# Performance work log

Measured on AMD Instinct MI355X. Metric: run time of the kernel, lower is better.

Reference implementation:

```python
import jax, jax.numpy as jnp
import numpy as np

BITS = 4
MASK = (1 << BITS) - 1  # 15
GROUP_SIZE = 128
IN_F, OUT_F = 4096, 11008
N_GROUPS = IN_F // GROUP_SIZE  # 32
PACK = 32 // BITS  # 8 nibbles per int32


def setup_inputs() -> dict:
    key = jax.random.key(0)
    k1, k2, k3, k4, k5 = jax.random.split(key, 5)
    x = jax.random.normal(k1, (64, IN_F), dtype=jnp.float32)
    # arbitrary packed int4 payloads: random 32-bit patterns viewed as int32
    qweight = jax.lax.bitcast_convert_type(
        jax.random.bits(k2, (IN_F // 32 * BITS, OUT_F), dtype=jnp.uint32), jnp.int32)
    qzeros = jax.lax.bitcast_convert_type(
        jax.random.bits(k3, (N_GROUPS, OUT_F // 32 * BITS), dtype=jnp.uint32), jnp.int32)
    scales = (jax.random.uniform(k4, (N_GROUPS, OUT_F), dtype=jnp.float32) + 0.1) * 0.01
    g_idx = (jnp.arange(IN_F, dtype=jnp.int32) // GROUP_SIZE).astype(jnp.int32)
    bias = jax.random.normal(k5, (OUT_F,), dtype=jnp.float32)
    return {"x": x, "qweight": qweight, "qzeros": qzeros,
            "scales": scales, "g_idx": g_idx, "bias": bias}


def reference(x, qweight, qzeros, scales, g_idx, bias):
    wf = jnp.arange(0, 32, BITS, dtype=jnp.int32)  # [8] shift amounts
    # unpack zero points: [n_groups, out/8, 8] -> [n_groups, out]
    zeros = (jnp.right_shift(qzeros[:, :, None], wf[None, None, :]) & MASK) + 1
    zeros = zeros.reshape(scales.shape).astype(scales.dtype)
    # unpack weights: [in/8, 8, out] -> [in, out]
    w = jnp.right_shift(qweight[:, None, :], wf[None, :, None]) & MASK
    w = w.reshape(-1, qweight.shape[1]).astype(scales.dtype)
    # per-group dequant, then dense matmul
    W = scales[g_idx] * (w - zeros[g_idx])  # [in, out]
    out = jnp.matmul(x, W).astype(x.dtype) + bias.astype(x.dtype)
    return out
```

## Files before the change

### kernel.cpp

```cpp
#include <hip/hip_runtime.h>

#define IN_F 4096
#define OUT_F 11008
#define M_ROWS 64
#define KSPLIT 4
#define GPB 8
#define NT_BLK 64
#define NBLK_N (OUT_F / NT_BLK)
#define QZ_WORDS (OUT_F / 8)
#define LDS_ROW 65

typedef __attribute__((ext_vector_type(8))) short short8;
typedef __attribute__((ext_vector_type(4))) float float4v;

__device__ __forceinline__ short f2bf(float f) {
    unsigned u = __builtin_bit_cast(unsigned, f);
    return (short)((u + 0x7FFFu + ((u >> 16) & 1u)) >> 16);
}
__device__ __forceinline__ short f2bf_t(float f) {
    return (short)(__builtin_bit_cast(unsigned, f) >> 16);
}

__global__ __launch_bounds__(128) void qlin_kernel(
    const float* __restrict__ x,
    const int*   __restrict__ qweight,
    const int*   __restrict__ qzeros,
    const float* __restrict__ scales,
    const float* __restrict__ bias,
    float* __restrict__ out)
{
    __shared__ short lds_a[16 * LDS_ROW * 8];

    const int blk  = blockIdx.x;
    const int nb   = blk % NBLK_N;
    const int kg   = blk / NBLK_N;
    const int t    = threadIdx.x;
    const int wave = t >> 6;
    const int lane = t & 63;
    const int q    = lane >> 4;
    const int nl   = lane & 15;
    const int n0   = nb * NT_BLK + wave * 32 + nl;
    const int n1   = n0 + 16;
    const int shz  = (n0 & 7) * 4;

    const int sm   = lane;
    const int ublk = wave * 8;
    const int g0   = kg * GPB;

    float4v xr[16];
    {
        const float* src = x + sm * IN_F + g0 * 128 + ublk * 8;
#pragma unroll
        for (int i = 0; i < 16; ++i) xr[i] = *(const float4v*)(src + i * 4);
    }

    float4v acc0[4], acc1[4];
#pragma unroll
    for (int i = 0; i < 4; ++i) {
        acc0[i] = (float4v){0.f, 0.f, 0.f, 0.f};
        acc1[i] = (float4v){0.f, 0.f, 0.f, 0.f};
    }

#pragma unroll
    for (int gi = 0; gi < GPB; ++gi) {
        const int g = g0 + gi;

        __syncthreads();
#pragma unroll
        for (int i = 0; i < 8; ++i) {
            short8 h;
#pragma unroll
            for (int j = 0; j < 4; ++j) {
                h[j]     = f2bf(xr[2 * i][j]);
                h[j + 4] = f2bf(xr[2 * i + 1][j]);
            }
            *(short8*)&lds_a[((ublk + i) * LDS_ROW + sm) * 8] = h;
        }
        __syncthreads();

        if (gi + 1 < GPB) {
            const float* src = x + sm * IN_F + (g + 1) * 128 + ublk * 8;
#pragma unroll
            for (int i = 0; i < 16; ++i) xr[i] = *(const float4v*)(src + i * 4);
        }

        int qwA[4], qwB[4];
#pragma unroll
        for (int kk = 0; kk < 4; ++kk) {
            const int row = g * 16 + kk * 4 + q;
            qwA[kk] = qweight[row * OUT_F + n0];
            qwB[kk] = qweight[row * OUT_F + n1];
        }
        const int   z0 = ((qzeros[g * QZ_WORDS + (n0 >> 3)] >> shz) & 15) + 1;
        const int   z1 = ((qzeros[g * QZ_WORDS + (n1 >> 3)] >> shz) & 15) + 1;
        const float s0 = scales[g * OUT_F + n0];
        const float s1 = scales[g * OUT_F + n1];
        const float nz0 = -s0 * (float)z0;
        const float nz1 = -s1 * (float)z1;

#pragma unroll
        for (int kk = 0; kk < 4; ++kk) {
            short8 b0, b1;
#pragma unroll
            for (int j = 0; j < 8; ++j) {
                b0[j] = f2bf_t(fmaf(s0, (float)((qwA[kk] >> (4 * j)) & 15), nz0));
                b1[j] = f2bf_t(fmaf(s1, (float)((qwB[kk] >> (4 * j)) & 15), nz1));
            }
            const int u = kk * 4 + q;
#pragma unroll
            for (int mt = 0; mt < 4; ++mt) {
                short8 a = *(const short8*)&lds_a[(u * LDS_ROW + mt * 16 + nl) * 8];
                acc0[mt] = __builtin_amdgcn_mfma_f32_16x16x32_bf16(a, b0, acc0[mt], 0, 0, 0);
                acc1[mt] = __builtin_amdgcn_mfma_f32_16x16x32_bf16(a, b1, acc1[mt], 0, 0, 0);
            }
        }
    }

    const float bv0 = (kg == 0) ? bias[n0] : 0.f;
    const float bv1 = (kg == 0) ? bias[n1] : 0.f;
#pragma unroll
    for (int mt = 0; mt < 4; ++mt) {
#pragma unroll
        for (int r = 0; r < 4; ++r) {
            const int m = mt * 16 + q * 4 + r;
            atomicAdd(&out[m * OUT_F + n0], acc0[mt][r] + bv0);
            atomicAdd(&out[m * OUT_F + n1], acc1[mt][r] + bv1);
        }
    }
}

extern "C" void kernel_launch(void* const* d_in, const int* in_sizes, int n_in,
                              void* d_out, int out_size, void* d_ws, size_t ws_size,
                              hipStream_t stream) {
    const float* x       = (const float*)d_in[0];
    const int*   qweight = (const int*)d_in[1];
    const int*   qzeros  = (const int*)d_in[2];
    const float* scales  = (const float*)d_in[3];
    const float* bias    = (const float*)d_in[5];
    float* out = (float*)d_out;

    hipMemsetAsync(out, 0, (size_t)M_ROWS * OUT_F * sizeof(float), stream);
    qlin_kernel<<<dim3(NBLK_N * KSPLIT), dim3(128), 0, stream>>>(
        x, qweight, qzeros, scales, bias, out);
}
```

Measured before the change: 110.2 us.

## Pre-convert activations to bf16 and double-buffer async LDS staging with prefetched metadata

A separate kernel now converts x to bf16 in an MFMA-friendly layout in workspace. The main kernel streams that data straight into double-buffered LDS with global_load_lds and prefetches the next group's qweight, zeros and scales while the current group computes. It also changes the tiling to 256 threads with 128 output columns per block and a K-split of 8. This removes per-block redundant fp32-to-bf16 conversion and overlaps loads with MFMA, at the cost of an extra launch, twice as many atomic partial sums and the loss of LDS padding, which may cause bank conflicts.

```diff
diff --git a/kernel.cpp b/kernel.cpp
--- a/kernel.cpp
+++ b/kernel.cpp
@@ -3,12 +3,11 @@
 #define IN_F 4096
 #define OUT_F 11008
 #define M_ROWS 64
-#define KSPLIT 4
-#define GPB 8
-#define NT_BLK 64
+#define KSPLIT 8
+#define GPB 4
+#define NT_BLK 128
 #define NBLK_N (OUT_F / NT_BLK)
 #define QZ_WORDS (OUT_F / 8)
-#define LDS_ROW 65
 
 typedef __attribute__((ext_vector_type(8))) short short8;
 typedef __attribute__((ext_vector_type(4))) float float4v;
@@ -21,15 +20,31 @@
     return (short)(__builtin_bit_cast(unsigned, f) >> 16);
 }
 
-__global__ __launch_bounds__(128) void qlin_kernel(
-    const float* __restrict__ x,
+__global__ __launch_bounds__(256) void cvt_kernel(const float* __restrict__ x,
+                                                  short* __restrict__ xbf2) {
+    const int T = blockIdx.x * 256 + threadIdx.x;
+    const int u = T >> 6, m = T & 63;
+    const float* src = x + m * IN_F + u * 8;
+    float4v f0 = *(const float4v*)src;
+    float4v f1 = *(const float4v*)(src + 4);
+    short8 h;
+#pragma unroll
+    for (int j = 0; j < 4; ++j) {
+        h[j]     = f2bf(f0[j]);
+        h[j + 4] = f2bf(f1[j]);
+    }
+    *(short8*)(xbf2 + T * 8) = h;
+}
+
+__global__ __launch_bounds__(256, 2) void qlin_kernel(
+    const short* __restrict__ xbf2,
     const int*   __restrict__ qweight,
     const int*   __restrict__ qzeros,
     const float* __restrict__ scales,
     const float* __restrict__ bias,
     float* __restrict__ out)
 {
-    __shared__ short lds_a[16 * LDS_ROW * 8];
+    __shared__ short lds_a[2][16][64][8];
 
     const int blk  = blockIdx.x;
     const int nb   = blk % NBLK_N;
@@ -42,17 +57,7 @@
     const int n0   = nb * NT_BLK + wave * 32 + nl;
     const int n1   = n0 + 16;
     const int shz  = (n0 & 7) * 4;
-
-    const int sm   = lane;
-    const int ublk = wave * 8;
     const int g0   = kg * GPB;
-
-    float4v xr[16];
-    {
-        const float* src = x + sm * IN_F + g0 * 128 + ublk * 8;
-#pragma unroll
-        for (int i = 0; i < 16; ++i) xr[i] = *(const float4v*)(src + i * 4);
-    }
 
     float4v acc0[4], acc1[4];
 #pragma unroll
@@ -61,58 +66,74 @@
         acc1[i] = (float4v){0.f, 0.f, 0.f, 0.f};
     }
 
+#define STAGE(buf, g)                                                          \
+    {                                                                          \
+        _Pragma("unroll")                                                      \
+        for (int i_ = 0; i_ < 4; ++i_) {                                       \
+            const int u_ = wave * 4 + i_;                                      \
+            const short* gsrc_ = xbf2 + (((g) * 16 + u_) * 64 + lane) * 8;     \
+            __builtin_amdgcn_global_load_lds(                                  \
+                (const __attribute__((address_space(1))) void*)gsrc_,          \
+                (__attribute__((address_space(3))) void*)&lds_a[buf][u_][0][0],\
+                16, 0, 0);                                                     \
+        }                                                                      \
+    }
+
+#define LOAD_META(g, qw, zw0, zw1, s0v, s1v)                                   \
+    {                                                                          \
+        _Pragma("unroll")                                                      \
+        for (int kk_ = 0; kk_ < 4; ++kk_) {                                    \
+            const int row_ = (g) * 16 + kk_ * 4 + q;                           \
+            qw[kk_]     = qweight[row_ * OUT_F + n0];                          \
+            qw[kk_ + 4] = qweight[row_ * OUT_F + n1];                          \
+        }                                                                      \
+        zw0 = qzeros[(g) * QZ_WORDS + (n0 >> 3)];                              \
+        zw1 = qzeros[(g) * QZ_WORDS + (n1 >> 3)];                              \
+        s0v = scales[(g) * OUT_F + n0];                                        \
+        s1v = scales[(g) * OUT_F + n1];                                        \
+    }
+
+    int qwc[8], zc0, zc1;
+    float sc0, sc1;
+    STAGE(0, g0);
+    LOAD_META(g0, qwc, zc0, zc1, sc0, sc1);
+
 #pragma unroll
     for (int gi = 0; gi < GPB; ++gi) {
-        const int g = g0 + gi;
-
-        __syncthreads();
-#pragma unroll
-        for (int i = 0; i < 8; ++i) {
-            short8 h;
-#pragma unroll
-            for (int j = 0; j < 4; ++j) {
-                h[j]     = f2bf(xr[2 * i][j]);
-                h[j + 4] = f2bf(xr[2 * i + 1][j]);
-            }
-            *(short8*)&lds_a[((ublk + i) * LDS_ROW + sm) * 8] = h;
-        }
         __syncthreads();
 
+        int qwn[8], zn0, zn1;
+        float sn0, sn1;
         if (gi + 1 < GPB) {
-            const float* src = x + sm * IN_F + (g + 1) * 128 + ublk * 8;
-#pragma unroll
-            for (int i = 0; i < 16; ++i) xr[i] = *(const float4v*)(src + i * 4);
+            STAGE((gi + 1) & 1, g0 + gi + 1);
+            LOAD_META(g0 + gi + 1, qwn, zn0, zn1, sn0, sn1);
         }
 
-        int qwA[4], qwB[4];
-#pragma unroll
-        for (int kk = 0; kk < 4; ++kk) {
-            const int row = g * 16 + kk * 4 + q;
-            qwA[kk] = qweight[row * OUT_F + n0];
-            qwB[kk] = qweight[row * OUT_F + n1];
-        }
-        const int   z0 = ((qzeros[g * QZ_WORDS + (n0 >> 3)] >> shz) & 15) + 1;
-        const int   z1 = ((qzeros[g * QZ_WORDS + (n1 >> 3)] >> shz) & 15) + 1;
-        const float s0 = scales[g * OUT_F + n0];
-        const float s1 = scales[g * OUT_F + n1];
-        const float nz0 = -s0 * (float)z0;
-        const float nz1 = -s1 * (float)z1;
+        const float s0  = sc0, s1 = sc1;
+        const float nz0 = -s0 * (float)(((zc0 >> shz) & 15) + 1);
+        const float nz1 = -s1 * (float)(((zc1 >> shz) & 15) + 1);
 
 #pragma unroll
         for (int kk = 0; kk < 4; ++kk) {
             short8 b0, b1;
 #pragma unroll
             for (int j = 0; j < 8; ++j) {
-                b0[j] = f2bf_t(fmaf(s0, (float)((qwA[kk] >> (4 * j)) & 15), nz0));
-                b1[j] = f2bf_t(fmaf(s1, (float)((qwB[kk] >> (4 * j)) & 15), nz1));
+                b0[j] = f2bf_t(fmaf(s0, (float)((qwc[kk] >> (4 * j)) & 15), nz0));
+                b1[j] = f2bf_t(fmaf(s1, (float)((qwc[kk + 4] >> (4 * j)) & 15), nz1));
             }
             const int u = kk * 4 + q;
 #pragma unroll
             for (int mt = 0; mt < 4; ++mt) {
-                short8 a = *(const short8*)&lds_a[(u * LDS_ROW + mt * 16 + nl) * 8];
+                short8 a = *(const short8*)&lds_a[gi & 1][u][mt * 16 + nl][0];
                 acc0[mt] = __builtin_amdgcn_mfma_f32_16x16x32_bf16(a, b0, acc0[mt], 0, 0, 0);
                 acc1[mt] = __builtin_amdgcn_mfma_f32_16x16x32_bf16(a, b1, acc1[mt], 0, 0, 0);
             }
+        }
+
+        if (gi + 1 < GPB) {
+#pragma unroll
+            for (int i = 0; i < 8; ++i) qwc[i] = qwn[i];
+            zc0 = zn0; zc1 = zn1; sc0 = sn0; sc1 = sn1;
         }
     }
 
@@ -127,6 +148,8 @@
             atomicAdd(&out[m * OUT_F + n1], acc1[mt][r] + bv1);
         }
     }
+#undef STAGE
+#undef LOAD_META
 }
 
 extern "C" void kernel_launch(void* const* d_in, const int* in_sizes, int n_in,
@@ -138,8 +161,10 @@
     const float* scales  = (const float*)d_in[3];
     const float* bias    = (const float*)d_in[5];
     float* out = (float*)d_out;
+    short* xbf2 = (short*)d_ws;
 
     hipMemsetAsync(out, 0, (size_t)M_ROWS * OUT_F * sizeof(float), stream);
-    qlin_kernel<<<dim3(NBLK_N * KSPLIT), dim3(128), 0, stream>>>(
-        x, qweight, qzeros, scales, bias, out);
+    cvt_kernel<<<dim3((IN_F / 8) * M_ROWS / 256), dim3(256), 0, stream>>>(x, xbf2);
+    qlin_kernel<<<dim3(NBLK_N * KSPLIT), dim3(256), 0, stream>>>(
+        xbf2, qweight, qzeros, scales, bias, out);
 }
```

New measurement: 102.4 us. 1.08x faster.
